# Kernel optimization log

Hardware: AMD Instinct MI355X
Metric: run time of the kernel (lower is better)

The kernel has to match this reference:

```python
import jax, jax.numpy as jnp
import numpy as np

B, D, K = 8192, 256, 65536  # batch, feature dim (layer_szs[0]), codebook size (layer_szs[1])
EPS = 1e-7


def setup_inputs() -> dict:
    key = jax.random.key(0)
    k1, k2 = jax.random.split(key)
    targ = jax.random.normal(k1, (B, D), dtype=jnp.float32)
    # learned codebook weights: nn.Linear(K, D).weight has shape [D, K]
    W = jax.random.normal(k2, (D, K), dtype=jnp.float32) * 0.02
    return {"targ": targ, "W": W}


def reference(targ, W):
    """MemUnit.recall with simFunc=1 (cosine similarity) and actFunc=0 (hard argmax).

    a[b,k] = <t[b], W[:,k]> / (||t[b]|| * ||W[:,k]|| + eps)   # infer_step
    z      = one_hot(argmax_k a)                                # hard assignment
    out    = z @ W.T  ==  W[:, argmax].T                        # predict (codebook gather)
    """
    t = targ.reshape(targ.shape[0], -1)                  # [B, D]
    row_nm = jnp.linalg.norm(t, axis=1)                  # [B]
    col_nm = jnp.linalg.norm(W, axis=0)                  # [K]
    a = (t @ W) / (row_nm[:, None] * col_nm[None, :] + EPS)  # [B, K] cosine sims
    idx = jnp.argmax(a, axis=1)                          # [B]
    # one-hot @ W.T is exactly a row-gather of the codebook
    return jnp.take(W, idx, axis=1).T                    # [B, D]
```

## Files before the change

kernel.cpp:

```cpp
#include <hip/hip_runtime.h>
#include <stdint.h>

#define B_N 8192
#define D_N 256
#define K_N 65536
#define EPS_ 1e-7f

#define T_SCALE 256.0f
#define W_SCALE 1024.0f
#define INV_SCALE (1.0f / 262144.0f)

typedef _Float16 half8 __attribute__((ext_vector_type(8)));
typedef _Float16 half4 __attribute__((ext_vector_type(4)));
typedef float f32x4 __attribute__((ext_vector_type(4)));

__device__ __forceinline__ unsigned long long pack_key(float v, uint32_t k) {
    uint32_t u = __float_as_uint(v);
    u = (u & 0x80000000u) ? ~u : (u | 0x80000000u);
    return ((unsigned long long)u << 32) | (unsigned long long)(~k);
}


__global__ void colnorm_init_kernel(const float* __restrict__ W, float* __restrict__ cn,
                                    unsigned long long* __restrict__ packed) {
    int k = blockIdx.x * blockDim.x + threadIdx.x;
    float s = 0.f;
#pragma unroll 8
    for (int d = 0; d < D_N; ++d) {
        float w = W[(size_t)d * K_N + k];
        s = fmaf(w, w, s);
    }
    cn[k] = sqrtf(s);
    if (k < B_N) packed[k] = 0ull;
}

__global__ void rownorm_kernel(const float* __restrict__ T, float* __restrict__ rn) {
    int row = blockIdx.x * 4 + (threadIdx.x >> 6);
    int lane = threadIdx.x & 63;
    float4 v = reinterpret_cast<const float4*>(T + (size_t)row * D_N)[lane];
    float s = v.x * v.x + v.y * v.y + v.z * v.z + v.w * v.w;
#pragma unroll
    for (int off = 32; off > 0; off >>= 1) s += __shfl_down(s, off);
    if (lane == 0) rn[row] = sqrtf(s);
}

__global__ void gather_kernel(const float* __restrict__ W,
                              const unsigned long long* __restrict__ packed,
                              float* __restrict__ out) {
    int b = blockIdx.x;
    int d = threadIdx.x;
    uint32_t idx = ~(uint32_t)(packed[b]);
    out[(size_t)b * D_N + d] = W[(size_t)d * K_N + idx];
}


__global__ void convT_kernel(const float* __restrict__ T,
                             _Float16* __restrict__ Ah, _Float16* __restrict__ Al) {
    int i = blockIdx.x * 256 + threadIdx.x;
    float4 v = reinterpret_cast<const float4*>(T)[i];
    float x[4] = {v.x, v.y, v.z, v.w};
    half4 hv, lv;
#pragma unroll
    for (int j = 0; j < 4; ++j) {
        float s = x[j] * T_SCALE;
        _Float16 h = (_Float16)s;
        hv[j] = h;
        lv[j] = (_Float16)(s - (float)h);
    }
    reinterpret_cast<half4*>(Ah)[i] = hv;
    reinterpret_cast<half4*>(Al)[i] = lv;
}

__global__ void convW_kernel(const float* __restrict__ W,
                             _Float16* __restrict__ Bh, _Float16* __restrict__ Bl) {
    __shared__ _Float16 Lh[64][66], Ll[64][66];
    int k0 = blockIdx.x * 64, d0 = blockIdx.y * 64;
    int t = threadIdx.x;
#pragma unroll
    for (int i = 0; i < 16; ++i) {
        int flat = i * 256 + t;
        int dl = flat >> 6, kl = flat & 63;
        float x = W[(size_t)(d0 + dl) * K_N + k0 + kl] * W_SCALE;
        _Float16 h = (_Float16)x;
        Lh[dl][kl] = h;
        Ll[dl][kl] = (_Float16)(x - (float)h);
    }
    __syncthreads();
#pragma unroll
    for (int j = 0; j < 2; ++j) {
        int flat = j * 256 + t;
        int kr = flat >> 3, seg = flat & 7;
        half8 vh, vl;
#pragma unroll
        for (int e = 0; e < 8; ++e) {
            vh[e] = Lh[seg * 8 + e][kr];
            vl[e] = Ll[seg * 8 + e][kr];
        }
        *reinterpret_cast<half8*>(Bh + (size_t)(k0 + kr) * D_N + d0 + seg * 8) = vh;
        *reinterpret_cast<half8*>(Bl + (size_t)(k0 + kr) * D_N + d0 + seg * 8) = vl;
    }
}


__device__ __forceinline__ void gload_lds16(const void* g, void* l) {
    __builtin_amdgcn_global_load_lds((const __attribute__((address_space(1))) unsigned int*)g,
                                     (__attribute__((address_space(3))) unsigned int*)l, 16, 0, 0);
}

#define NCHUNK 24

__launch_bounds__(256) __global__
void fused_mfma_kernel(const _Float16* __restrict__ Ah, const _Float16* __restrict__ Al,
                       const _Float16* __restrict__ Bh, const _Float16* __restrict__ Bl,
                       const float* __restrict__ rn, const float* __restrict__ cn,
                       unsigned long long* __restrict__ packed) {
    __shared__ _Float16 As[2][128][32];
    __shared__ _Float16 Bs[2][128][32];

    const int tid = threadIdx.x;
    const int lane = tid & 63, wid = tid >> 6;
    const int wr = wid >> 1, wc = wid & 1;

    const uint32_t linear = blockIdx.x + 64u * blockIdx.y;
    const uint32_t swz = (linear & 7u) * 4096u + (linear >> 3);
    const int r0 = (int)(swz & 63u) * 128;
    const int c0 = (int)(swz >> 6) * 128;

    f32x4 acc[4][4];
#pragma unroll
    for (int i = 0; i < 4; ++i)
#pragma unroll
        for (int j = 0; j < 4; ++j) acc[i][j] = (f32x4){0.f, 0.f, 0.f, 0.f};

    const int lrow = lane >> 2, lcol = (lane & 3) * 8;
    const int frow = lane & 15, fk = (lane >> 4) * 8;

    auto stage = [&](int ch, int buf) {
        const int term = ch >> 3;
        const int d0 = (ch & 7) << 5;
        const _Float16* Asrc = (term == 1) ? Al : Ah;
        const _Float16* Bsrc = (term == 2) ? Bl : Bh;
        const _Float16* ga = Asrc + (size_t)(r0 + wid * 16 + lrow) * D_N + d0 + lcol;
        gload_lds16(ga,            &As[buf][wid * 16][0]);
        gload_lds16(ga + 64 * D_N, &As[buf][64 + wid * 16][0]);
        const _Float16* gb = Bsrc + (size_t)(c0 + wid * 16 + lrow) * D_N + d0 + lcol;
        gload_lds16(gb,            &Bs[buf][wid * 16][0]);
        gload_lds16(gb + 64 * D_N, &Bs[buf][64 + wid * 16][0]);
    };

    stage(0, 0);
    __syncthreads();

    int cur = 0;
    for (int ch = 0; ch < NCHUNK; ++ch) {
        if (ch + 1 < NCHUNK) stage(ch + 1, cur ^ 1);

        half8 a[4], b[4];
#pragma unroll
        for (int mi = 0; mi < 4; ++mi)
            a[mi] = *reinterpret_cast<const half8*>(&As[cur][wr * 64 + mi * 16 + frow][fk]);
#pragma unroll
        for (int ni = 0; ni < 4; ++ni)
            b[ni] = *reinterpret_cast<const half8*>(&Bs[cur][wc * 64 + ni * 16 + frow][fk]);
#pragma unroll
        for (int mi = 0; mi < 4; ++mi)
#pragma unroll
            for (int ni = 0; ni < 4; ++ni)
                acc[mi][ni] = __builtin_amdgcn_mfma_f32_16x16x32_f16(a[mi], b[ni], acc[mi][ni], 0, 0, 0);

        __syncthreads();
        cur ^= 1;
    }

    const int q = lane >> 4;
    const int cl = lane & 15;
    float cns[4];
#pragma unroll
    for (int ni = 0; ni < 4; ++ni) cns[ni] = cn[c0 + wc * 64 + ni * 16 + cl];

#pragma unroll
    for (int mi = 0; mi < 4; ++mi) {
#pragma unroll
        for (int reg = 0; reg < 4; ++reg) {
            const int row = r0 + wr * 64 + mi * 16 + q * 4 + reg;
            const float rv = rn[row];
            unsigned long long key = 0ull;
#pragma unroll
            for (int ni = 0; ni < 4; ++ni) {
                float v = acc[mi][ni][reg] * INV_SCALE / (rv * cns[ni] + EPS_);
                unsigned long long cand = pack_key(v, (uint32_t)(c0 + wc * 64 + ni * 16 + cl));
                key = cand > key ? cand : key;
            }
#pragma unroll
            for (int m = 1; m <= 8; m <<= 1) {
                uint32_t lo = (uint32_t)key, hi = (uint32_t)(key >> 32);
                lo = __shfl_xor(lo, m);
                hi = __shfl_xor(hi, m);
                unsigned long long o = ((unsigned long long)hi << 32) | (unsigned long long)lo;
                key = o > key ? o : key;
            }
            if (cl == 0) atomicMax(&packed[row], key);
        }
    }
}


#define TM 128
#define TN 128
#define DK 32
#define LDT 132

__launch_bounds__(256) __global__
void fused_sim_argmax_kernel(const float* __restrict__ T, const float* __restrict__ W,
                             const float* __restrict__ rn, const float* __restrict__ cn,
                             unsigned long long* __restrict__ packed) {
    __shared__ __align__(16) float As[DK][LDT];
    __shared__ __align__(16) float Ws[DK][LDT];
    const int tid = threadIdx.x;
    const int tx = tid & 15, ty = tid >> 4;
    const int r0 = blockIdx.y * TM, c0 = blockIdx.x * TN;
    float acc[8][8] = {};
    for (int d0 = 0; d0 < D_N; d0 += DK) {
#pragma unroll
        for (int t = 0; t < 4; ++t) {
            int fidx = tid + t * 256;
            int r = fidx >> 3, dq = fidx & 7;
            float4 v = *reinterpret_cast<const float4*>(T + (size_t)(r0 + r) * D_N + d0 + dq * 4);
            As[dq * 4 + 0][r] = v.x; As[dq * 4 + 1][r] = v.y;
            As[dq * 4 + 2][r] = v.z; As[dq * 4 + 3][r] = v.w;
        }
#pragma unroll
        for (int t = 0; t < 4; ++t) {
            int fidx = tid + t * 256;
            int dd = fidx >> 5, c4 = fidx & 31;
            float4 v = *reinterpret_cast<const float4*>(W + (size_t)(d0 + dd) * K_N + c0 + c4 * 4);
            *reinterpret_cast<float4*>(&Ws[dd][c4 * 4]) = v;
        }
        __syncthreads();
#pragma unroll 8
        for (int dd = 0; dd < DK; ++dd) {
            float a[8], w[8];
            *reinterpret_cast<float4*>(&a[0]) = *reinterpret_cast<const float4*>(&As[dd][ty * 8]);
            *reinterpret_cast<float4*>(&a[4]) = *reinterpret_cast<const float4*>(&As[dd][ty * 8 + 4]);
            *reinterpret_cast<float4*>(&w[0]) = *reinterpret_cast<const float4*>(&Ws[dd][tx * 8]);
            *reinterpret_cast<float4*>(&w[4]) = *reinterpret_cast<const float4*>(&Ws[dd][tx * 8 + 4]);
#pragma unroll
            for (int i = 0; i < 8; ++i)
#pragma unroll
                for (int j = 0; j < 8; ++j) acc[i][j] = fmaf(a[i], w[j], acc[i][j]);
        }
        __syncthreads();
    }
    float rns[8], cns[8];
#pragma unroll
    for (int i = 0; i < 8; ++i) rns[i] = rn[r0 + ty * 8 + i];
#pragma unroll
    for (int j = 0; j < 8; ++j) cns[j] = cn[c0 + tx * 8 + j];
#pragma unroll
    for (int i = 0; i < 8; ++i) {
        unsigned long long key = 0ull;
#pragma unroll
        for (int j = 0; j < 8; ++j) {
            float v = acc[i][j] / (rns[i] * cns[j] + EPS_);
            unsigned long long cand = pack_key(v, (uint32_t)(c0 + tx * 8 + j));
            key = cand > key ? cand : key;
        }
#pragma unroll
        for (int m = 1; m <= 8; m <<= 1) {
            uint32_t lo = (uint32_t)key, hi = (uint32_t)(key >> 32);
            lo = __shfl_xor(lo, m); hi = __shfl_xor(hi, m);
            unsigned long long o = ((unsigned long long)hi << 32) | (unsigned long long)lo;
            key = o > key ? o : key;
        }
        if (tx == 0) atomicMax(&packed[r0 + ty * 8 + i], key);
    }
}


extern "C" void kernel_launch(void* const* d_in, const int* in_sizes, int n_in,
                              void* d_out, int out_size, void* d_ws, size_t ws_size,
                              hipStream_t stream) {
    const float* T = (const float*)d_in[0];
    const float* W = (const float*)d_in[1];
    float* out = (float*)d_out;

    const size_t BH_OFF = 0;
    const size_t BL_OFF = BH_OFF + (size_t)K_N * D_N * 2;
    const size_t AH_OFF = BL_OFF + (size_t)K_N * D_N * 2;
    const size_t AL_OFF = AH_OFF + (size_t)B_N * D_N * 2;
    const size_t CN_OFF = AL_OFF + (size_t)B_N * D_N * 2;
    const size_t RN_OFF = CN_OFF + (size_t)K_N * 4;
    const size_t PK_OFF = RN_OFF + (size_t)B_N * 4;
    const size_t NEED = PK_OFF + (size_t)B_N * 8;

    char* ws = (char*)d_ws;

    if (ws_size >= NEED) {
        _Float16* Bh = (_Float16*)(ws + BH_OFF);
        _Float16* Bl = (_Float16*)(ws + BL_OFF);
        _Float16* Ah = (_Float16*)(ws + AH_OFF);
        _Float16* Al = (_Float16*)(ws + AL_OFF);
        float* cn = (float*)(ws + CN_OFF);
        float* rn = (float*)(ws + RN_OFF);
        unsigned long long* packed = (unsigned long long*)(ws + PK_OFF);

        colnorm_init_kernel<<<K_N / 256, 256, 0, stream>>>(W, cn, packed);
        rownorm_kernel<<<B_N / 4, 256, 0, stream>>>(T, rn);
        convT_kernel<<<B_N * D_N / 4 / 256, 256, 0, stream>>>(T, Ah, Al);
        dim3 gw(K_N / 64, D_N / 64);
        convW_kernel<<<gw, 256, 0, stream>>>(W, Bh, Bl);

        dim3 grid(64, 512);
        fused_mfma_kernel<<<grid, 256, 0, stream>>>(Ah, Al, Bh, Bl, rn, cn, packed);

        gather_kernel<<<B_N, 256, 0, stream>>>(W, packed, out);
    } else {
        float* cn = (float*)ws;
        float* rn = cn + K_N;
        unsigned long long* packed = (unsigned long long*)(rn + B_N);
        colnorm_init_kernel<<<K_N / 256, 256, 0, stream>>>(W, cn, packed);
        rownorm_kernel<<<B_N / 4, 256, 0, stream>>>(T, rn);
        dim3 grid(K_N / TN, B_N / TM);
        fused_sim_argmax_kernel<<<grid, 256, 0, stream>>>(T, W, rn, cn, packed);
        gather_kernel<<<B_N, 256, 0, stream>>>(W, packed, out);
    }
}
```

Before: 1.544 ms.

## Triple-buffer LDS staging with XOR swizzle and explicit vmcnt waits in MFMA GEMM

Replaces the double-buffered LDS pipeline with a three-stage ring that prefetches two chunks ahead. Fine-grained s_waitcnt vmcnt waits plus raw s_barrier replace __syncthreads, so global loads stay in flight across iterations. An XOR swizzle on the LDS column layout is meant to reduce bank conflicts on fragment reads. Launch bounds now request 3 blocks per CU, which adds register pressure and uses more LDS per block.

Result: faster. 1.502 ms (-2.7%).

```diff
diff --git a/kernel.cpp b/kernel.cpp
--- a/kernel.cpp
+++ b/kernel.cpp
@@ -102,20 +102,20 @@
 }
 
 
-__device__ __forceinline__ void gload_lds16(const void* g, void* l) {
+__device__ __forceinline__ void gload_lds16(const _Float16* g, _Float16* l) {
     __builtin_amdgcn_global_load_lds((const __attribute__((address_space(1))) unsigned int*)g,
                                      (__attribute__((address_space(3))) unsigned int*)l, 16, 0, 0);
 }
 
 #define NCHUNK 24
 
-__launch_bounds__(256) __global__
+__launch_bounds__(256, 3) __global__
 void fused_mfma_kernel(const _Float16* __restrict__ Ah, const _Float16* __restrict__ Al,
                        const _Float16* __restrict__ Bh, const _Float16* __restrict__ Bl,
                        const float* __restrict__ rn, const float* __restrict__ cn,
                        unsigned long long* __restrict__ packed) {
-    __shared__ _Float16 As[2][128][32];
-    __shared__ _Float16 Bs[2][128][32];
+    __shared__ _Float16 sA[3 * 128 * 32];
+    __shared__ _Float16 sB[3 * 128 * 32];
 
     const int tid = threadIdx.x;
     const int lane = tid & 63, wid = tid >> 6;
@@ -132,45 +132,63 @@
 #pragma unroll
         for (int j = 0; j < 4; ++j) acc[i][j] = (f32x4){0.f, 0.f, 0.f, 0.f};
 
-    const int lrow = lane >> 2, lcol = (lane & 3) * 8;
-    const int frow = lane & 15, fk = (lane >> 4) * 8;
-
-    auto stage = [&](int ch, int buf) {
-        const int term = ch >> 3;
-        const int d0 = (ch & 7) << 5;
-        const _Float16* Asrc = (term == 1) ? Al : Ah;
-        const _Float16* Bsrc = (term == 2) ? Bl : Bh;
-        const _Float16* ga = Asrc + (size_t)(r0 + wid * 16 + lrow) * D_N + d0 + lcol;
-        gload_lds16(ga,            &As[buf][wid * 16][0]);
-        gload_lds16(ga + 64 * D_N, &As[buf][64 + wid * 16][0]);
-        const _Float16* gb = Bsrc + (size_t)(c0 + wid * 16 + lrow) * D_N + d0 + lcol;
-        gload_lds16(gb,            &Bs[buf][wid * 16][0]);
-        gload_lds16(gb + 64 * D_N, &Bs[buf][64 + wid * 16][0]);
-    };
-
-    stage(0, 0);
-    __syncthreads();
-
-    int cur = 0;
+    const int srow = lane >> 2;
+    const int scol = ((lane & 3) ^ ((lane >> 3) & 3)) * 8;
+    const _Float16* pAh = Ah + (size_t)(r0 + wid * 16 + srow) * D_N + scol;
+    const _Float16* pAl = Al + (size_t)(r0 + wid * 16 + srow) * D_N + scol;
+    const _Float16* pBh = Bh + (size_t)(c0 + wid * 16 + srow) * D_N + scol;
+    const _Float16* pBl = Bl + (size_t)(c0 + wid * 16 + srow) * D_N + scol;
+    _Float16* ldsA = sA + wid * 512;
+    _Float16* ldsB = sB + wid * 512;
+
+    const int frow = lane & 15;
+    const int fkp = ((lane >> 4) ^ ((frow >> 1) & 3)) * 8;
+    const _Float16* rA = sA + (wr * 64 + frow) * 32 + fkp;
+    const _Float16* rB = sB + (wc * 64 + frow) * 32 + fkp;
+
+#define STAGE(ch, b) {                                                        \
+        const _Float16* pa = (((ch) >> 3) == 1) ? pAl : pAh;                  \
+        const _Float16* pb = (((ch) >> 3) == 2) ? pBl : pBh;                  \
+        const int dd = ((ch) & 7) * 32;                                       \
+        gload_lds16(pa + dd,             ldsA + (b) * 4096);                  \
+        gload_lds16(pa + dd + 64 * D_N,  ldsA + (b) * 4096 + 2048);           \
+        gload_lds16(pb + dd,             ldsB + (b) * 4096);                  \
+        gload_lds16(pb + dd + 64 * D_N,  ldsB + (b) * 4096 + 2048);           \
+    }
+
+    STAGE(0, 0);
+    STAGE(1, 1);
+
+#pragma unroll
     for (int ch = 0; ch < NCHUNK; ++ch) {
-        if (ch + 1 < NCHUNK) stage(ch + 1, cur ^ 1);
-
-        half8 a[4], b[4];
+        const int b = ch % 3;
+        if (ch + 2 < NCHUNK) STAGE(ch + 2, (ch + 2) % 3);
+
+        if (ch < NCHUNK - 2)       asm volatile("s_waitcnt vmcnt(8)" ::: "memory");
+        else if (ch == NCHUNK - 2) asm volatile("s_waitcnt vmcnt(4)" ::: "memory");
+        else                       asm volatile("s_waitcnt vmcnt(0)" ::: "memory");
+        __builtin_amdgcn_s_barrier();
+        __builtin_amdgcn_sched_barrier(0);
+
+        const _Float16* rAb = rA + b * 4096;
+        const _Float16* rBb = rB + b * 4096;
+        half8 a[4], bf[4];
 #pragma unroll
         for (int mi = 0; mi < 4; ++mi)
-            a[mi] = *reinterpret_cast<const half8*>(&As[cur][wr * 64 + mi * 16 + frow][fk]);
+            a[mi] = *reinterpret_cast<const half8*>(rAb + mi * 512);
 #pragma unroll
         for (int ni = 0; ni < 4; ++ni)
-            b[ni] = *reinterpret_cast<const half8*>(&Bs[cur][wc * 64 + ni * 16 + frow][fk]);
+            bf[ni] = *reinterpret_cast<const half8*>(rBb + ni * 512);
 #pragma unroll
         for (int mi = 0; mi < 4; ++mi)
 #pragma unroll
             for (int ni = 0; ni < 4; ++ni)
-                acc[mi][ni] = __builtin_amdgcn_mfma_f32_16x16x32_f16(a[mi], b[ni], acc[mi][ni], 0, 0, 0);
-
-        __syncthreads();
-        cur ^= 1;
-    }
+                acc[mi][ni] = __builtin_amdgcn_mfma_f32_16x16x32_f16(a[mi], bf[ni], acc[mi][ni], 0, 0, 0);
+
+        __builtin_amdgcn_sched_barrier(0);
+        __builtin_amdgcn_s_barrier();
+    }
+#undef STAGE
 
     const int q = lane >> 4;
     const int cl = lane & 15;
```
